# Kernel optimization log

Measured on AMD Instinct MI355X. Metric: run time of the kernel, lower is better.

The kernel has to match this reference:

```python
import jax, jax.numpy as jnp
import numpy as np

N = 50000      # nodes
E = 800000     # edges
XS = 64        # x_size
ES = 32        # edge_attr dim (in_size = XS + ES = 96)
OUT = 64       # out_size
H = 128        # hidden_size
EPS = 1e-5


def _lin_init(k, fan_in, fan_out):
    s = 1.0 / np.sqrt(fan_in)
    kw, kb = jax.random.split(k)
    w = jax.random.uniform(kw, (fan_in, fan_out), minval=-s, maxval=s, dtype=jnp.float32)
    b = jax.random.uniform(kb, (fan_out,), minval=-s, maxval=s, dtype=jnp.float32)
    return w, b


def setup_inputs() -> dict:
    key = jax.random.key(0)
    ks = jax.random.split(key, 12)
    x = jax.random.normal(ks[0], (N, XS), dtype=jnp.float32)
    edge_index = jax.random.randint(ks[1], (2, E), 0, N, dtype=jnp.int64)
    edge_attr = jax.random.normal(ks[2], (E, ES), dtype=jnp.float32)
    u = jax.random.normal(ks[3], (1, 8), dtype=jnp.float32)
    batch = jnp.zeros((N,), dtype=jnp.int64)
    # MLP1: (96->128) LReLU (128->128) LReLU (128->64) LReLU LN(64)
    m1w0, m1b0 = _lin_init(ks[4], XS + ES, H)
    m1w1, m1b1 = _lin_init(ks[5], H, H)
    m1w2, m1b2 = _lin_init(ks[6], H, OUT)
    ln1_g = jnp.ones((OUT,), jnp.float32); ln1_b = jnp.zeros((OUT,), jnp.float32)
    # MLP2: (128->128) LReLU (128->128) LReLU (128->64) LReLU LN(64)
    m2w0, m2b0 = _lin_init(ks[7], XS + OUT, H)
    m2w1, m2b1 = _lin_init(ks[8], H, H)
    m2w2, m2b2 = _lin_init(ks[9], H, OUT)
    ln2_g = jnp.ones((OUT,), jnp.float32); ln2_b = jnp.zeros((OUT,), jnp.float32)
    return dict(x=x, edge_index=edge_index, edge_attr=edge_attr, u=u, batch=batch,
                m1w0=m1w0, m1b0=m1b0, m1w1=m1w1, m1b1=m1b1, m1w2=m1w2, m1b2=m1b2,
                ln1_g=ln1_g, ln1_b=ln1_b,
                m2w0=m2w0, m2b0=m2b0, m2w1=m2w1, m2b1=m2b1, m2w2=m2w2, m2b2=m2b2,
                ln2_g=ln2_g, ln2_b=ln2_b)


def _lrelu(v):
    return jax.nn.leaky_relu(v, 0.01)


def _layernorm(v, g, b):
    mu = jnp.mean(v, axis=-1, keepdims=True)
    var = jnp.mean(jnp.square(v - mu), axis=-1, keepdims=True)
    return (v - mu) * jax.lax.rsqrt(var + EPS) * g + b


def _mlp(h, w0, b0, w1, b1, w2, b2, g, bn):
    h = _lrelu(h @ w0 + b0)
    h = _lrelu(h @ w1 + b1)
    h = _lrelu(h @ w2 + b2)          # activate_last=True
    return _layernorm(h, g, bn)      # layer_norm=True


def reference(x, edge_index, edge_attr, u, batch,
              m1w0, m1b0, m1w1, m1b1, m1w2, m1b2, ln1_g, ln1_b,
              m2w0, m2b0, m2w1, m2b1, m2w2, m2b2, ln2_g, ln2_b):
    row, col = edge_index[0], edge_index[1]
    # gather source nodes, concat edge features -> per-edge MLP
    h = jnp.concatenate([x[row], edge_attr], axis=1)            # [E, 96]
    h = _mlp(h, m1w0, m1b0, m1w1, m1b1, m1w2, m1b2, ln1_g, ln1_b)  # [E, 64]
    # scatter_mean over destination nodes
    agg = jax.ops.segment_sum(h, col, num_segments=N)           # [N, 64]
    cnt = jax.ops.segment_sum(jnp.ones((E,), h.dtype), col, num_segments=N)
    agg = agg / jnp.maximum(cnt, 1.0)[:, None]
    # node update MLP
    h2 = jnp.concatenate([x, agg], axis=1)                      # [N, 128]
    return _mlp(h2, m2w0, m2b0, m2w1, m2b1, m2w2, m2b2, ln2_g, ln2_b)
```

## Files before the change

kernel.cpp:

```cpp
#include <hip/hip_runtime.h>


#define NNODES 50000
#define NEDGES 800000
#define NTILES_E 6250
#define NTILES_N 391

typedef __bf16 bf16;
typedef __bf16 __attribute__((ext_vector_type(4))) bf16x4;
typedef __bf16 __attribute__((ext_vector_type(8))) bf16x8;
typedef float __attribute__((ext_vector_type(4))) f32x4;

__device__ __forceinline__ f32x4 mfma_bf16(bf16x8 a, bf16x8 b, f32x4 c) {
    return __builtin_amdgcn_mfma_f32_16x16x32_bf16(a, b, c, 0, 0, 0);
}

__global__ void prep_weights(const float* __restrict__ w10, const float* __restrict__ w11,
                             const float* __restrict__ w12, const float* __restrict__ w20,
                             const float* __restrict__ w21, const float* __restrict__ w22,
                             bf16* __restrict__ img) {
    int idx = blockIdx.x * 256 + threadIdx.x;
    float f;
    if (idx < 13312) {
        int n = idx / 104, k = idx % 104;
        f = (k < 96) ? w10[k * 128 + n] : 0.0f;
    } else if (idx < 30720) {
        int t = idx - 13312; int n = t / 136, k = t % 136;
        f = (k < 128) ? w11[k * 128 + n] : 0.0f;
    } else if (idx < 39424) {
        int t = idx - 30720; int n = t / 136, k = t % 136;
        f = (k < 128) ? w12[k * 64 + n] : 0.0f;
    } else if (idx < 56832) {
        int t = idx - 39424; int n = t / 136, k = t % 136;
        f = (k < 128) ? w20[k * 128 + n] : 0.0f;
    } else if (idx < 74240) {
        int t = idx - 56832; int n = t / 136, k = t % 136;
        f = (k < 128) ? w21[k * 128 + n] : 0.0f;
    } else if (idx < 82944) {
        int t = idx - 74240; int n = t / 136, k = t % 136;
        f = (k < 128) ? w22[k * 64 + n] : 0.0f;
    } else {
        return;
    }
    img[idx] = (bf16)f;
}

__global__ void hist_kernel(const int* __restrict__ col, int* __restrict__ hist) {
    int i = blockIdx.x * 512 + threadIdx.x;
    if (i < NEDGES) {
        int d = col[i];
        if ((unsigned)d < (unsigned)NNODES) atomicAdd(hist + d, 1);
    }
}

__global__ void scanA(const int* __restrict__ hist, int* __restrict__ off,
                      int* __restrict__ csum) {
    __shared__ int sd[512];
    int t = threadIdx.x, i = blockIdx.x * 512 + t;
    int v = (i < NNODES) ? hist[i] : 0;
    sd[t] = v;
    __syncthreads();
    for (int o2 = 1; o2 < 512; o2 <<= 1) {
        int x = (t >= o2) ? sd[t - o2] : 0;
        __syncthreads();
        sd[t] += x;
        __syncthreads();
    }
    if (i < NNODES) off[i] = sd[t] - v;
    if (t == 511) csum[blockIdx.x] = sd[511];
}

__global__ void scanB(int* __restrict__ csum) {
    __shared__ int sd[128];
    int t = threadIdx.x;
    int v = (t < 98) ? csum[t] : 0;
    sd[t] = v;
    __syncthreads();
    for (int o2 = 1; o2 < 128; o2 <<= 1) {
        int x = (t >= o2) ? sd[t - o2] : 0;
        __syncthreads();
        sd[t] += x;
        __syncthreads();
    }
    if (t < 98) csum[t] = sd[t] - v;
}

__global__ void scanC(int* __restrict__ off, const int* __restrict__ csum) {
    int i = blockIdx.x * 512 + threadIdx.x;
    if (i < NNODES) off[i] += csum[blockIdx.x];
}

__global__ void scatter_kernel(const int* __restrict__ eidx, int* __restrict__ off,
                               int* __restrict__ perm, int* __restrict__ rdS) {
    int i = blockIdx.x * 512 + threadIdx.x;
    if (i < NEDGES) {
        int r = eidx[i], d = eidx[NEDGES + i];
        if ((unsigned)d < (unsigned)NNODES && (unsigned)r < (unsigned)NNODES) {
            int pos = atomicAdd(off + d, 1);
            if ((unsigned)pos < (unsigned)NEDGES) {
                perm[pos] = i;
                rdS[pos] = (int)(((unsigned)r & 0xFFFFu) | ((unsigned)d << 16));
            }
        }
    }
}

__global__ __launch_bounds__(256) void edge_mlp(
    const float* __restrict__ x, const int* __restrict__ perm,
    const int* __restrict__ rdS, const float* __restrict__ eattr,
    const bf16* __restrict__ wimg,
    const float* __restrict__ b0g, const float* __restrict__ b1g,
    const float* __restrict__ b2g, const float* __restrict__ lng,
    const float* __restrict__ lnb, float* __restrict__ agg) {
    __shared__ __align__(16) bf16 buf[128 * 136];
    __shared__ float bs[448];
    __shared__ int dstile[128];

    const int tid = threadIdx.x;
    if (tid < 128) { bs[tid] = b0g[tid]; bs[128 + tid] = b1g[tid]; }
    else {
        int t = tid - 128;
        if (t < 64) { bs[256 + t] = b2g[t]; bs[320 + t] = lng[t]; bs[384 + t] = lnb[t]; }
    }
    __syncthreads();

    const int lane = tid & 63;
    const int wv = tid >> 6;
    const int col16 = lane & 15;
    const int quad = lane >> 4;

    float b0r[8], b1r[8], b2r[4], gr[4], br[4];
#pragma unroll
    for (int i = 0; i < 8; i++) { b0r[i] = bs[i * 16 + col16]; b1r[i] = bs[128 + i * 16 + col16]; }
#pragma unroll
    for (int i = 0; i < 4; i++) {
        b2r[i] = bs[256 + i * 16 + col16];
        gr[i] = bs[320 + i * 16 + col16];
        br[i] = bs[384 + i * 16 + col16];
    }

    const bf16* w0t = wimg;
    const bf16* w1t = wimg + 13312;
    const bf16* w2t = wimg + 30720;

    const f32x4 vzero = {0.0f, 0.0f, 0.0f, 0.0f};
    const int r0 = wv * 32 + col16;
    const int rw = wv * 32 + quad * 4;
    const int el = tid >> 1, half = tid & 1;

    for (int tile = blockIdx.x; tile < NTILES_E; tile += gridDim.x) {
        const int sbase = tile * 128;
        {
            const int s = sbase + el;
            const unsigned v = (unsigned)rdS[s];
            int e = perm[s];
            int r = (int)(v & 0xFFFFu);
            unsigned d = v >> 16;
            if (r >= NNODES) r = 0;
            if ((unsigned)e >= (unsigned)NEDGES) e = 0;
            if (half == 0) dstile[el] = (d < (unsigned)NNODES) ? (int)d : 0;
            const float4* xs = (const float4*)(x + (size_t)r * 64);
            bf16* arow = buf + el * 136;
#pragma unroll
            for (int j = 0; j < 8; j++) {
                float4 vv = xs[half * 8 + j];
                bf16x4 u = {(bf16)vv.x, (bf16)vv.y, (bf16)vv.z, (bf16)vv.w};
                *(bf16x4*)(arow + half * 32 + j * 4) = u;
            }
            const float4* es = (const float4*)(eattr + (size_t)e * 32);
#pragma unroll
            for (int j = 0; j < 4; j++) {
                float4 vv = es[half * 4 + j];
                bf16x4 u = {(bf16)vv.x, (bf16)vv.y, (bf16)vv.z, (bf16)vv.w};
                *(bf16x4*)(arow + 64 + half * 16 + j * 4) = u;
            }
        }
        __syncthreads();

        f32x4 acc1[2][8];
#pragma unroll
        for (int mt = 0; mt < 2; mt++)
#pragma unroll
            for (int nt = 0; nt < 8; nt++) acc1[mt][nt] = vzero;
#pragma unroll
        for (int ks = 0; ks < 3; ks++) {
            bf16x8 a0 = *(const bf16x8*)(buf + r0 * 136 + ks * 32 + quad * 8);
            bf16x8 a1 = *(const bf16x8*)(buf + (r0 + 16) * 136 + ks * 32 + quad * 8);
#pragma unroll
            for (int nt = 0; nt < 8; nt++) {
                bf16x8 b = *(const bf16x8*)(w0t + (nt * 16 + col16) * 104 + ks * 32 + quad * 8);
                acc1[0][nt] = mfma_bf16(a0, b, acc1[0][nt]);
                acc1[1][nt] = mfma_bf16(a1, b, acc1[1][nt]);
            }
        }
#pragma unroll
        for (int mt = 0; mt < 2; mt++)
#pragma unroll
            for (int nt = 0; nt < 8; nt++)
#pragma unroll
                for (int rg = 0; rg < 4; rg++) {
                    float v = acc1[mt][nt][rg] + b0r[nt];
                    v = (v > 0.0f) ? v : 0.01f * v;
                    buf[(rw + mt * 16 + rg) * 136 + nt * 16 + col16] = (bf16)v;
                }

        bf16x8 a2[2][4];
#pragma unroll
        for (int mt = 0; mt < 2; mt++)
#pragma unroll
            for (int ks = 0; ks < 4; ks++)
                a2[mt][ks] = *(const bf16x8*)(buf + (r0 + mt * 16) * 136 + ks * 32 + quad * 8);
        f32x4 acc2[2][8];
#pragma unroll
        for (int mt = 0; mt < 2; mt++)
#pragma unroll
            for (int nt = 0; nt < 8; nt++) acc2[mt][nt] = vzero;
#pragma unroll
        for (int ks = 0; ks < 4; ks++) {
#pragma unroll
            for (int nt = 0; nt < 8; nt++) {
                bf16x8 b = *(const bf16x8*)(w1t + (nt * 16 + col16) * 136 + ks * 32 + quad * 8);
                acc2[0][nt] = mfma_bf16(a2[0][ks], b, acc2[0][nt]);
                acc2[1][nt] = mfma_bf16(a2[1][ks], b, acc2[1][nt]);
            }
        }
#pragma unroll
        for (int mt = 0; mt < 2; mt++)
#pragma unroll
            for (int nt = 0; nt < 8; nt++)
#pragma unroll
                for (int rg = 0; rg < 4; rg++) {
                    float v = acc2[mt][nt][rg] + b1r[nt];
                    v = (v > 0.0f) ? v : 0.01f * v;
                    buf[(rw + mt * 16 + rg) * 136 + nt * 16 + col16] = (bf16)v;
                }

        bf16x8 a3[2][4];
#pragma unroll
        for (int mt = 0; mt < 2; mt++)
#pragma unroll
            for (int ks = 0; ks < 4; ks++)
                a3[mt][ks] = *(const bf16x8*)(buf + (r0 + mt * 16) * 136 + ks * 32 + quad * 8);
        f32x4 acc3[2][4];
#pragma unroll
        for (int mt = 0; mt < 2; mt++)
#pragma unroll
            for (int nt = 0; nt < 4; nt++) acc3[mt][nt] = vzero;
#pragma unroll
        for (int ks = 0; ks < 4; ks++) {
#pragma unroll
            for (int nt = 0; nt < 4; nt++) {
                bf16x8 b = *(const bf16x8*)(w2t + (nt * 16 + col16) * 136 + ks * 32 + quad * 8);
                acc3[0][nt] = mfma_bf16(a3[0][ks], b, acc3[0][nt]);
                acc3[1][nt] = mfma_bf16(a3[1][ks], b, acc3[1][nt]);
            }
        }

#pragma unroll
        for (int mt = 0; mt < 2; mt++) {
            float vals[4][4];
            float s1[4] = {0.f, 0.f, 0.f, 0.f}, s2[4] = {0.f, 0.f, 0.f, 0.f};
#pragma unroll
            for (int nt = 0; nt < 4; nt++)
#pragma unroll
                for (int rg = 0; rg < 4; rg++) {
                    float v = acc3[mt][nt][rg] + b2r[nt];
                    v = (v > 0.0f) ? v : 0.01f * v;
                    vals[nt][rg] = v;
                    s1[rg] += v;
                    s2[rg] += v * v;
                }
#pragma unroll
            for (int off2 = 1; off2 < 16; off2 <<= 1) {
#pragma unroll
                for (int rg = 0; rg < 4; rg++) {
                    s1[rg] += __shfl_xor(s1[rg], off2);
                    s2[rg] += __shfl_xor(s2[rg], off2);
                }
            }
            float o[4][4];
            int dr[4];
#pragma unroll
            for (int rg = 0; rg < 4; rg++) {
                float mu = s1[rg] * 0.015625f;
                float var = s2[rg] * 0.015625f - mu * mu;
                float rstd = rsqrtf(var + 1e-5f);
                int c = dstile[rw + mt * 16 + rg];
                dr[rg] = ((unsigned)c < (unsigned)NNODES) ? c : 0;
#pragma unroll
                for (int nt = 0; nt < 4; nt++)
                    o[nt][rg] = (vals[nt][rg] - mu) * rstd * gr[nt] + br[nt];
            }
            float run0 = o[0][0], run1 = o[1][0], run2 = o[2][0], run3 = o[3][0];
            int cur = dr[0];
#pragma unroll
            for (int rg = 1; rg < 4; rg++) {
                if (dr[rg] != cur) {
                    float* dst = agg + (size_t)cur * 64 + col16;
                    atomicAdd(dst, run0); atomicAdd(dst + 16, run1);
                    atomicAdd(dst + 32, run2); atomicAdd(dst + 48, run3);
                    run0 = o[0][rg]; run1 = o[1][rg]; run2 = o[2][rg]; run3 = o[3][rg];
                    cur = dr[rg];
                } else {
                    run0 += o[0][rg]; run1 += o[1][rg]; run2 += o[2][rg]; run3 += o[3][rg];
                }
            }
            float* dst = agg + (size_t)cur * 64 + col16;
            atomicAdd(dst, run0); atomicAdd(dst + 16, run1);
            atomicAdd(dst + 32, run2); atomicAdd(dst + 48, run3);
        }
        __syncthreads();
    }
}

__global__ __launch_bounds__(256) void node_mlp(
    const float* __restrict__ x, const float* __restrict__ agg,
    const int* __restrict__ hist, const bf16* __restrict__ wimg,
    const float* __restrict__ b0g, const float* __restrict__ b1g,
    const float* __restrict__ b2g, const float* __restrict__ lng,
    const float* __restrict__ lnb, float* __restrict__ out) {
    __shared__ __align__(16) bf16 buf[128 * 136];
    __shared__ float bs[448];

    const int tid = threadIdx.x;
    if (tid < 128) { bs[tid] = b0g[tid]; bs[128 + tid] = b1g[tid]; }
    else {
        int t = tid - 128;
        if (t < 64) { bs[256 + t] = b2g[t]; bs[320 + t] = lng[t]; bs[384 + t] = lnb[t]; }
    }
    __syncthreads();

    const int lane = tid & 63;
    const int wv = tid >> 6;
    const int col16 = lane & 15;
    const int quad = lane >> 4;

    float b0r[8], b1r[8], b2r[4], gr[4], br[4];
#pragma unroll
    for (int i = 0; i < 8; i++) { b0r[i] = bs[i * 16 + col16]; b1r[i] = bs[128 + i * 16 + col16]; }
#pragma unroll
    for (int i = 0; i < 4; i++) {
        b2r[i] = bs[256 + i * 16 + col16];
        gr[i] = bs[320 + i * 16 + col16];
        br[i] = bs[384 + i * 16 + col16];
    }

    const bf16* w0t = wimg;
    const bf16* w1t = wimg + 17408;
    const bf16* w2t = wimg + 34816;

    const f32x4 vzero = {0.0f, 0.0f, 0.0f, 0.0f};
    const int r0 = wv * 32 + col16;
    const int rw = wv * 32 + quad * 4;
    const int el = tid >> 1, half = tid & 1;

    for (int tile = blockIdx.x; tile < NTILES_N; tile += gridDim.x) {
        const int nbase = tile * 128;
        {
            int i = nbase + el;
            if (i >= NNODES) i = NNODES - 1;
            const float4* xs = (const float4*)(x + (size_t)i * 64);
            bf16* arow = buf + el * 136;
#pragma unroll
            for (int j = 0; j < 8; j++) {
                float4 v = xs[half * 8 + j];
                bf16x4 u = {(bf16)v.x, (bf16)v.y, (bf16)v.z, (bf16)v.w};
                *(bf16x4*)(arow + half * 32 + j * 4) = u;
            }
            int c = hist[i];
            float inv = 1.0f / (float)(c > 1 ? c : 1);
            const float4* as = (const float4*)(agg + (size_t)i * 64);
#pragma unroll
            for (int j = 0; j < 8; j++) {
                float4 v = as[half * 8 + j];
                bf16x4 u = {(bf16)(v.x * inv), (bf16)(v.y * inv), (bf16)(v.z * inv), (bf16)(v.w * inv)};
                *(bf16x4*)(arow + 64 + half * 32 + j * 4) = u;
            }
        }
        __syncthreads();

        f32x4 acc1[2][8];
#pragma unroll
        for (int mt = 0; mt < 2; mt++)
#pragma unroll
            for (int nt = 0; nt < 8; nt++) acc1[mt][nt] = vzero;
#pragma unroll
        for (int ks = 0; ks < 4; ks++) {
            bf16x8 a0 = *(const bf16x8*)(buf + r0 * 136 + ks * 32 + quad * 8);
            bf16x8 a1 = *(const bf16x8*)(buf + (r0 + 16) * 136 + ks * 32 + quad * 8);
#pragma unroll
            for (int nt = 0; nt < 8; nt++) {
                bf16x8 b = *(const bf16x8*)(w0t + (nt * 16 + col16) * 136 + ks * 32 + quad * 8);
                acc1[0][nt] = mfma_bf16(a0, b, acc1[0][nt]);
                acc1[1][nt] = mfma_bf16(a1, b, acc1[1][nt]);
            }
        }
#pragma unroll
        for (int mt = 0; mt < 2; mt++)
#pragma unroll
            for (int nt = 0; nt < 8; nt++)
#pragma unroll
                for (int rg = 0; rg < 4; rg++) {
                    float v = acc1[mt][nt][rg] + b0r[nt];
                    v = (v > 0.0f) ? v : 0.01f * v;
                    buf[(rw + mt * 16 + rg) * 136 + nt * 16 + col16] = (bf16)v;
                }

        bf16x8 a2[2][4];
#pragma unroll
        for (int mt = 0; mt < 2; mt++)
#pragma unroll
            for (int ks = 0; ks < 4; ks++)
                a2[mt][ks] = *(const bf16x8*)(buf + (r0 + mt * 16) * 136 + ks * 32 + quad * 8);
        f32x4 acc2[2][8];
#pragma unroll
        for (int mt = 0; mt < 2; mt++)
#pragma unroll
            for (int nt = 0; nt < 8; nt++) acc2[mt][nt] = vzero;
#pragma unroll
        for (int ks = 0; ks < 4; ks++) {
#pragma unroll
            for (int nt = 0; nt < 8; nt++) {
                bf16x8 b = *(const bf16x8*)(w1t + (nt * 16 + col16) * 136 + ks * 32 + quad * 8);
                acc2[0][nt] = mfma_bf16(a2[0][ks], b, acc2[0][nt]);
                acc2[1][nt] = mfma_bf16(a2[1][ks], b, acc2[1][nt]);
            }
        }
#pragma unroll
        for (int mt = 0; mt < 2; mt++)
#pragma unroll
            for (int nt = 0; nt < 8; nt++)
#pragma unroll
                for (int rg = 0; rg < 4; rg++) {
                    float v = acc2[mt][nt][rg] + b1r[nt];
                    v = (v > 0.0f) ? v : 0.01f * v;
                    buf[(rw + mt * 16 + rg) * 136 + nt * 16 + col16] = (bf16)v;
                }

        bf16x8 a3[2][4];
#pragma unroll
        for (int mt = 0; mt < 2; mt++)
#pragma unroll
            for (int ks = 0; ks < 4; ks++)
                a3[mt][ks] = *(const bf16x8*)(buf + (r0 + mt * 16) * 136 + ks * 32 + quad * 8);
        f32x4 acc3[2][4];
#pragma unroll
        for (int mt = 0; mt < 2; mt++)
#pragma unroll
            for (int nt = 0; nt < 4; nt++) acc3[mt][nt] = vzero;
#pragma unroll
        for (int ks = 0; ks < 4; ks++) {
#pragma unroll
            for (int nt = 0; nt < 4; nt++) {
                bf16x8 b = *(const bf16x8*)(w2t + (nt * 16 + col16) * 136 + ks * 32 + quad * 8);
                acc3[0][nt] = mfma_bf16(a3[0][ks], b, acc3[0][nt]);
                acc3[1][nt] = mfma_bf16(a3[1][ks], b, acc3[1][nt]);
            }
        }

#pragma unroll
        for (int mt = 0; mt < 2; mt++) {
            float vals[4][4];
            float s1[4] = {0.f, 0.f, 0.f, 0.f}, s2[4] = {0.f, 0.f, 0.f, 0.f};
#pragma unroll
            for (int nt = 0; nt < 4; nt++)
#pragma unroll
                for (int rg = 0; rg < 4; rg++) {
                    float v = acc3[mt][nt][rg] + b2r[nt];
                    v = (v > 0.0f) ? v : 0.01f * v;
                    vals[nt][rg] = v;
                    s1[rg] += v;
                    s2[rg] += v * v;
                }
#pragma unroll
            for (int off2 = 1; off2 < 16; off2 <<= 1) {
#pragma unroll
                for (int rg = 0; rg < 4; rg++) {
                    s1[rg] += __shfl_xor(s1[rg], off2);
                    s2[rg] += __shfl_xor(s2[rg], off2);
                }
            }
#pragma unroll
            for (int rg = 0; rg < 4; rg++) {
                float mu = s1[rg] * 0.015625f;
                float var = s2[rg] * 0.015625f - mu * mu;
                float rstd = rsqrtf(var + 1e-5f);
                int i = nbase + rw + mt * 16 + rg;
                if (i < NNODES) {
#pragma unroll
                    for (int nt = 0; nt < 4; nt++) {
                        float o = (vals[nt][rg] - mu) * rstd * gr[nt] + br[nt];
                        out[(size_t)i * 64 + nt * 16 + col16] = o;
                    }
                }
            }
        }
        __syncthreads();
    }
}

extern "C" void kernel_launch(void* const* d_in, const int* in_sizes, int n_in,
                              void* d_out, int out_size, void* d_ws, size_t ws_size,
                              hipStream_t stream) {
    (void)in_sizes; (void)n_in; (void)out_size; (void)ws_size;
    const float* x     = (const float*)d_in[0];
    const int*   eidx  = (const int*)d_in[1];
    const float* eattr = (const float*)d_in[2];
    const float* m1w0 = (const float*)d_in[5];
    const float* m1b0 = (const float*)d_in[6];
    const float* m1w1 = (const float*)d_in[7];
    const float* m1b1 = (const float*)d_in[8];
    const float* m1w2 = (const float*)d_in[9];
    const float* m1b2 = (const float*)d_in[10];
    const float* ln1g = (const float*)d_in[11];
    const float* ln1b = (const float*)d_in[12];
    const float* m2w0 = (const float*)d_in[13];
    const float* m2b0 = (const float*)d_in[14];
    const float* m2w1 = (const float*)d_in[15];
    const float* m2b1 = (const float*)d_in[16];
    const float* m2w2 = (const float*)d_in[17];
    const float* m2b2 = (const float*)d_in[18];
    const float* ln2g = (const float*)d_in[19];
    const float* ln2b = (const float*)d_in[20];

    char* ws = (char*)d_ws;
    float* agg  = (float*)ws;
    int*   hist = (int*)(ws + 12800000);
    int*   off  = (int*)(ws + 13000000);
    int*   csum = (int*)(ws + 13200000);
    int*   perm = (int*)(ws + 13200512);
    int*   rdS  = (int*)(ws + 16400512);
    bf16*  wimg = (bf16*)(ws + 19600512);

    hipMemsetAsync(d_ws, 0, 13000000, stream);
    prep_weights<<<324, 256, 0, stream>>>(m1w0, m1w1, m1w2, m2w0, m2w1, m2w2, wimg);
    hist_kernel<<<1563, 512, 0, stream>>>(eidx + NEDGES, hist);
    scanA<<<98, 512, 0, stream>>>(hist, off, csum);
    scanB<<<1, 128, 0, stream>>>(csum);
    scanC<<<98, 512, 0, stream>>>(off, csum);
    scatter_kernel<<<1563, 512, 0, stream>>>(eidx, off, perm, rdS);
    edge_mlp<<<1250, 256, 0, stream>>>(x, perm, rdS, eattr, wimg, m1b0, m1b1, m1b2,
                                       ln1g, ln1b, agg);
    node_mlp<<<391, 256, 0, stream>>>(x, agg, hist, wimg + 39424,
                                      m2b0, m2b1, m2b2, ln2g, ln2b, (float*)d_out);
}
```

Before: 592.3 us.

## Stage weights in LDS, double tile size, and prefetch next tile gathers

Both MLP kernels now copy the bf16 weight image into shared memory once per block and read B operands from LDS instead of global memory. Tiles grow to 256 rows with 512-thread blocks, and the grid shrinks to a persistent 256 (edge) or 196 (node) blocks. The next tile's gathered x/edge_attr rows and the index entries two tiles ahead are loaded into registers while the current tile's MFMAs run, hiding gather latency. The costs are more registers and LDS per block (about 150KB), which can lower occupancy, and fewer blocks to spread load across CUs.

```diff
diff --git a/kernel.cpp b/kernel.cpp
--- a/kernel.cpp
+++ b/kernel.cpp
@@ -3,8 +3,8 @@
 
 #define NNODES 50000
 #define NEDGES 800000
-#define NTILES_E 6250
-#define NTILES_N 391
+#define NTILES_E2 3125
+#define NTILES_N2 196
 
 typedef __bf16 bf16;
 typedef __bf16 __attribute__((ext_vector_type(4))) bf16x4;
@@ -105,22 +105,28 @@
     }
 }
 
-__global__ __launch_bounds__(256) void edge_mlp(
+__global__ __launch_bounds__(512, 2) void edge_mlp(
     const float* __restrict__ x, const int* __restrict__ perm,
     const int* __restrict__ rdS, const float* __restrict__ eattr,
     const bf16* __restrict__ wimg,
     const float* __restrict__ b0g, const float* __restrict__ b1g,
     const float* __restrict__ b2g, const float* __restrict__ lng,
     const float* __restrict__ lnb, float* __restrict__ agg) {
-    __shared__ __align__(16) bf16 buf[128 * 136];
+    __shared__ __align__(16) bf16 wall[39424];
+    __shared__ __align__(16) bf16 buf[256 * 136];
     __shared__ float bs[448];
-    __shared__ int dstile[128];
+    __shared__ int dstile[256];
 
     const int tid = threadIdx.x;
+    {
+        const uint4* src = (const uint4*)wimg;
+        uint4* dst = (uint4*)wall;
+        for (int i = tid; i < 4928; i += 512) dst[i] = src[i];
+    }
     if (tid < 128) { bs[tid] = b0g[tid]; bs[128 + tid] = b1g[tid]; }
-    else {
+    else if (tid < 192) {
         int t = tid - 128;
-        if (t < 64) { bs[256 + t] = b2g[t]; bs[320 + t] = lng[t]; bs[384 + t] = lnb[t]; }
+        bs[256 + t] = b2g[t]; bs[320 + t] = lng[t]; bs[384 + t] = lnb[t];
     }
     __syncthreads();
 
@@ -139,43 +145,81 @@
         br[i] = bs[384 + i * 16 + col16];
     }
 
-    const bf16* w0t = wimg;
-    const bf16* w1t = wimg + 13312;
-    const bf16* w2t = wimg + 30720;
+    const bf16* w0t = wall;
+    const bf16* w1t = wall + 13312;
+    const bf16* w2t = wall + 30720;
 
     const f32x4 vzero = {0.0f, 0.0f, 0.0f, 0.0f};
     const int r0 = wv * 32 + col16;
     const int rw = wv * 32 + quad * 4;
     const int el = tid >> 1, half = tid & 1;
-
-    for (int tile = blockIdx.x; tile < NTILES_E; tile += gridDim.x) {
-        const int sbase = tile * 128;
+    const int G = gridDim.x;
+
+    int tile = blockIdx.x;
+
+    float4 xr[8], er[4];
+    unsigned cv;
+    {
+        int s = tile * 256 + el;
+        cv = (unsigned)rdS[s];
+        int ce = perm[s];
+        int r = (int)(cv & 0xFFFFu); if (r >= NNODES) r = 0;
+        if ((unsigned)ce >= (unsigned)NEDGES) ce = 0;
+        const float4* xs = (const float4*)(x + (size_t)r * 64) + half * 8;
+        const float4* es = (const float4*)(eattr + (size_t)ce * 32) + half * 4;
+#pragma unroll
+        for (int j = 0; j < 8; j++) xr[j] = xs[j];
+#pragma unroll
+        for (int j = 0; j < 4; j++) er[j] = es[j];
+    }
+    unsigned nv; int ne;
+    {
+        int t1 = tile + G;
+        int s = (t1 < NTILES_E2 ? t1 * 256 : 0) + el;
+        nv = (unsigned)rdS[s];
+        ne = perm[s];
+    }
+
+    for (; tile < NTILES_E2; tile += G) {
         {
-            const int s = sbase + el;
-            const unsigned v = (unsigned)rdS[s];
-            int e = perm[s];
-            int r = (int)(v & 0xFFFFu);
-            unsigned d = v >> 16;
-            if (r >= NNODES) r = 0;
-            if ((unsigned)e >= (unsigned)NEDGES) e = 0;
+            unsigned d = cv >> 16;
             if (half == 0) dstile[el] = (d < (unsigned)NNODES) ? (int)d : 0;
-            const float4* xs = (const float4*)(x + (size_t)r * 64);
             bf16* arow = buf + el * 136;
 #pragma unroll
             for (int j = 0; j < 8; j++) {
-                float4 vv = xs[half * 8 + j];
+                float4 vv = xr[j];
                 bf16x4 u = {(bf16)vv.x, (bf16)vv.y, (bf16)vv.z, (bf16)vv.w};
                 *(bf16x4*)(arow + half * 32 + j * 4) = u;
             }
-            const float4* es = (const float4*)(eattr + (size_t)e * 32);
 #pragma unroll
             for (int j = 0; j < 4; j++) {
-                float4 vv = es[half * 4 + j];
+                float4 vv = er[j];
                 bf16x4 u = {(bf16)vv.x, (bf16)vv.y, (bf16)vv.z, (bf16)vv.w};
                 *(bf16x4*)(arow + 64 + half * 16 + j * 4) = u;
             }
         }
         __syncthreads();
+
+        {
+            int t2 = tile + G;
+            if (t2 < NTILES_E2) {
+                int r = (int)(nv & 0xFFFFu); if (r >= NNODES) r = 0;
+                int e = ne; if ((unsigned)e >= (unsigned)NEDGES) e = 0;
+                const float4* xs = (const float4*)(x + (size_t)r * 64) + half * 8;
+                const float4* es = (const float4*)(eattr + (size_t)e * 32) + half * 4;
+#pragma unroll
+                for (int j = 0; j < 8; j++) xr[j] = xs[j];
+#pragma unroll
+                for (int j = 0; j < 4; j++) er[j] = es[j];
+            }
+        }
+        unsigned pv; int pe;
+        {
+            int t3 = tile + 2 * G;
+            int s = (t3 < NTILES_E2 ? t3 * 256 : 0) + el;
+            pv = (unsigned)rdS[s];
+            pe = perm[s];
+        }
 
         f32x4 acc1[2][8];
 #pragma unroll
@@ -255,6 +299,16 @@
                 acc3[1][nt] = mfma_bf16(a3[1][ks], b, acc3[1][nt]);
             }
         }
+
+        int drA[2][4];
+#pragma unroll
+        for (int mt = 0; mt < 2; mt++)
+#pragma unroll
+            for (int rg = 0; rg < 4; rg++) {
+                int c = dstile[rw + mt * 16 + rg];
+                drA[mt][rg] = ((unsigned)c < (unsigned)NNODES) ? c : 0;
+            }
+        __syncthreads();
 
 #pragma unroll
         for (int mt = 0; mt < 2; mt++) {
@@ -279,28 +333,25 @@
                 }
             }
             float o[4][4];
-            int dr[4];
 #pragma unroll
             for (int rg = 0; rg < 4; rg++) {
                 float mu = s1[rg] * 0.015625f;
                 float var = s2[rg] * 0.015625f - mu * mu;
                 float rstd = rsqrtf(var + 1e-5f);
-                int c = dstile[rw + mt * 16 + rg];
-                dr[rg] = ((unsigned)c < (unsigned)NNODES) ? c : 0;
 #pragma unroll
                 for (int nt = 0; nt < 4; nt++)
                     o[nt][rg] = (vals[nt][rg] - mu) * rstd * gr[nt] + br[nt];
             }
             float run0 = o[0][0], run1 = o[1][0], run2 = o[2][0], run3 = o[3][0];
-            int cur = dr[0];
+            int cur = drA[mt][0];
 #pragma unroll
             for (int rg = 1; rg < 4; rg++) {
-                if (dr[rg] != cur) {
+                if (drA[mt][rg] != cur) {
                     float* dst = agg + (size_t)cur * 64 + col16;
                     atomicAdd(dst, run0); atomicAdd(dst + 16, run1);
                     atomicAdd(dst + 32, run2); atomicAdd(dst + 48, run3);
                     run0 = o[0][rg]; run1 = o[1][rg]; run2 = o[2][rg]; run3 = o[3][rg];
-                    cur = dr[rg];
+                    cur = drA[mt][rg];
                 } else {
                     run0 += o[0][rg]; run1 += o[1][rg]; run2 += o[2][rg]; run3 += o[3][rg];
                 }
@@ -309,24 +360,31 @@
             atomicAdd(dst, run0); atomicAdd(dst + 16, run1);
             atomicAdd(dst + 32, run2); atomicAdd(dst + 48, run3);
         }
-        __syncthreads();
-    }
-}
-
-__global__ __launch_bounds__(256) void node_mlp(
+
+        cv = nv; nv = pv; ne = pe;
+    }
+}
+
+__global__ __launch_bounds__(512, 2) void node_mlp(
     const float* __restrict__ x, const float* __restrict__ agg,
     const int* __restrict__ hist, const bf16* __restrict__ wimg,
     const float* __restrict__ b0g, const float* __restrict__ b1g,
     const float* __restrict__ b2g, const float* __restrict__ lng,
     const float* __restrict__ lnb, float* __restrict__ out) {
-    __shared__ __align__(16) bf16 buf[128 * 136];
+    __shared__ __align__(16) bf16 wall[43520];
+    __shared__ __align__(16) bf16 buf[256 * 136];
     __shared__ float bs[448];
 
     const int tid = threadIdx.x;
+    {
+        const uint4* src = (const uint4*)wimg;
+        uint4* dst = (uint4*)wall;
+        for (int i = tid; i < 5440; i += 512) dst[i] = src[i];
+    }
     if (tid < 128) { bs[tid] = b0g[tid]; bs[128 + tid] = b1g[tid]; }
-    else {
+    else if (tid < 192) {
         int t = tid - 128;
-        if (t < 64) { bs[256 + t] = b2g[t]; bs[320 + t] = lng[t]; bs[384 + t] = lnb[t]; }
+        bs[256 + t] = b2g[t]; bs[320 + t] = lng[t]; bs[384 + t] = lnb[t];
     }
     __syncthreads();
 
@@ -345,39 +403,63 @@
         br[i] = bs[384 + i * 16 + col16];
     }
 
-    const bf16* w0t = wimg;
-    const bf16* w1t = wimg + 17408;
-    const bf16* w2t = wimg + 34816;
+    const bf16* w0t = wall;
+    const bf16* w1t = wall + 17408;
+    const bf16* w2t = wall + 34816;
 
     const f32x4 vzero = {0.0f, 0.0f, 0.0f, 0.0f};
     const int r0 = wv * 32 + col16;
     const int rw = wv * 32 + quad * 4;
     const int el = tid >> 1, half = tid & 1;
-
-    for (int tile = blockIdx.x; tile < NTILES_N; tile += gridDim.x) {
-        const int nbase = tile * 128;
+    const int G = gridDim.x;
+
+    int tile = blockIdx.x;
+    if (tile >= NTILES_N2) return;
+
+    float4 xr[8], ar[8];
+    int cc;
+    {
+        int i = tile * 256 + el;
+        if (i >= NNODES) i = NNODES - 1;
+        const float4* xs = (const float4*)(x + (size_t)i * 64) + half * 8;
+        const float4* as = (const float4*)(agg + (size_t)i * 64) + half * 8;
+#pragma unroll
+        for (int j = 0; j < 8; j++) { xr[j] = xs[j]; ar[j] = as[j]; }
+        cc = hist[i];
+    }
+
+    for (; tile < NTILES_N2; tile += G) {
+        const int nbase = tile * 256;
         {
-            int i = nbase + el;
-            if (i >= NNODES) i = NNODES - 1;
-            const float4* xs = (const float4*)(x + (size_t)i * 64);
+            float inv = 1.0f / (float)(cc > 1 ? cc : 1);
             bf16* arow = buf + el * 136;
 #pragma unroll
             for (int j = 0; j < 8; j++) {
-                float4 v = xs[half * 8 + j];
+                float4 v = xr[j];
                 bf16x4 u = {(bf16)v.x, (bf16)v.y, (bf16)v.z, (bf16)v.w};
                 *(bf16x4*)(arow + half * 32 + j * 4) = u;
             }
-            int c = hist[i];
-            float inv = 1.0f / (float)(c > 1 ? c : 1);
-            const float4* as = (const float4*)(agg + (size_t)i * 64);
 #pragma unroll
             for (int j = 0; j < 8; j++) {
-                float4 v = as[half * 8 + j];
+                float4 v = ar[j];
                 bf16x4 u = {(bf16)(v.x * inv), (bf16)(v.y * inv), (bf16)(v.z * inv), (bf16)(v.w * inv)};
                 *(bf16x4*)(arow + 64 + half * 32 + j * 4) = u;
             }
         }
         __syncthreads();
+
+        {
+            int t2 = tile + G;
+            if (t2 < NTILES_N2) {
+                int i = t2 * 256 + el;
+                if (i >= NNODES) i = NNODES - 1;
+                const float4* xs = (const float4*)(x + (size_t)i * 64) + half * 8;
+                const float4* as = (const float4*)(agg + (size_t)i * 64) + half * 8;
+#pragma unroll
+                for (int j = 0; j < 8; j++) { xr[j] = xs[j]; ar[j] = as[j]; }
+                cc = hist[i];
+            }
+        }
 
         f32x4 acc1[2][8];
 #pragma unroll
@@ -457,6 +539,7 @@
                 acc3[1][nt] = mfma_bf16(a3[1][ks], b, acc3[1][nt]);
             }
         }
+        __syncthreads();
 
 #pragma unroll
         for (int mt = 0; mt < 2; mt++) {
@@ -495,7 +578,6 @@
                 }
             }
         }
-        __syncthreads();
     }
 }
 
@@ -539,8 +621,8 @@
     scanB<<<1, 128, 0, stream>>>(csum);
     scanC<<<98, 512, 0, stream>>>(off, csum);
     scatter_kernel<<<1563, 512, 0, stream>>>(eidx, off, perm, rdS);
-    edge_mlp<<<1250, 256, 0, stream>>>(x, perm, rdS, eattr, wimg, m1b0, m1b1, m1b2,
-                                       ln1g, ln1b, agg);
-    node_mlp<<<391, 256, 0, stream>>>(x, agg, hist, wimg + 39424,
+    edge_mlp<<<256, 512, 0, stream>>>(x, perm, rdS, eattr, wimg, m1b0, m1b1, m1b2,
+                                      ln1g, ln1b, agg);
+    node_mlp<<<196, 512, 0, stream>>>(x, agg, hist, wimg + 39424,
                                       m2b0, m2b1, m2b2, ln2g, ln2b, (float*)d_out);
 }
```

Measured after the change: 489.6 us. 17.3% less time.
